# Performance work log

Hardware: AMD Instinct MI355X
Metric: run time of the kernel (lower is better)

## Reference

```python
import jax, jax.numpy as jnp
import numpy as np

E, D, H, K, DIL, T = 8, 768, 3072, 3, 1, 16384


def _conv1d(x, w, b, dilation):
    # x: [1, C_in, L]; w: [C_out, C_in, K]; torch Conv1d with SAME padding
    pad = dilation * (w.shape[-1] - 1) // 2
    y = jax.lax.conv_general_dilated(
        x, w, window_strides=(1,), padding=[(pad, pad)],
        rhs_dilation=(dilation,), dimension_numbers=("NCH", "OIH", "NCH"))
    return y + b[None, :, None]


def setup_inputs() -> dict:
    key = jax.random.key(0)
    k0, k1, k2, k3, k4 = jax.random.split(key, 5)
    inp = jax.random.normal(k0, (T, D), dtype=jnp.float32)
    fwd_expert_count = jnp.full((E,), T // E, dtype=jnp.int32)
    w1 = jax.random.normal(k1, (E, H, D, K), dtype=jnp.float32) * (1.0 / np.sqrt(D * K))
    b1 = jax.random.normal(k2, (E, H), dtype=jnp.float32) * 0.01
    w2 = jax.random.normal(k3, (E, D, H, K), dtype=jnp.float32) * (1.0 / np.sqrt(H * K))
    b2 = jax.random.normal(k4, (E, D), dtype=jnp.float32) * 0.01
    return {"inp": inp, "fwd_expert_count": fwd_expert_count,
            "w1": w1, "b1": b1, "w2": w2, "b2": b2}


def reference(inp, fwd_expert_count, w1, b1, w2, b2):
    # counts define static per-expert segment lengths (constants w.r.t. compute graph)
    counts = np.asarray(jax.device_get(fwd_expert_count))
    x = inp.T[None]  # [1, D, T]
    outs, idx = [], 0
    for i in range(counts.shape[0]):
        n = int(counts[i])
        if n > 0:
            outs.append(_conv1d(x[:, :, idx:idx + n], w1[i], b1[i], DIL))
            idx += n
    h = jax.nn.gelu(jnp.concatenate(outs, axis=2), approximate=False)  # [1, H, T]
    outs, idx = [], 0
    for i in range(counts.shape[0]):
        n = int(counts[i])
        if n > 0:
            outs.append(_conv1d(h[:, :, idx:idx + n], w2[i], b2[i], DIL))
            idx += n
    y = jnp.concatenate(outs, axis=2)[0]  # [D, T]
    return y.T  # [T, D]
```

## Files before the change

### kernel.cpp

```cpp
#include <hip/hip_runtime.h>
#include <hip/hip_bf16.h>
#include <cstdint>

#define E_   8
#define D_   768
#define H_   3072
#define T_   16384
#define SEG  2048
#define PSEG (SEG + 2)

typedef __attribute__((ext_vector_type(8))) __bf16 bf16x8;
typedef __attribute__((ext_vector_type(4))) float f32x4;
typedef __attribute__((ext_vector_type(4))) unsigned int u32x4;

__device__ inline unsigned short f2bf(float f) {
  union { float f; unsigned int u; } v; v.f = f;
  unsigned int u = v.u;
  u += 0x7fffu + ((u >> 16) & 1u);
  return (unsigned short)(u >> 16);
}

__device__ inline float gelu_fast(float x) {
  const float a = -2.302118131f;
  const float b = -0.102944213f;
  float z = x * __builtin_fmaf(b, x * x, a);
  float e = __builtin_amdgcn_exp2f(z);
  return x * __builtin_amdgcn_rcpf(1.0f + e);
}

__device__ inline void gload16(const unsigned short* g, unsigned short* l) {
  __builtin_amdgcn_global_load_lds(
      (const __attribute__((address_space(1))) unsigned int*)g,
      (__attribute__((address_space(3))) unsigned int*)l, 16, 0, 0);
}

__global__ __launch_bounds__(256) void cvt_x_pad_kernel(const float* __restrict__ in,
                                                        unsigned short* __restrict__ out) {
  const int i = blockIdx.x * 256 + threadIdx.x;
  const int elem = i * 8;
  const int row = elem / D_;
  const int col = elem - row * D_;
  const int prow = (row >> 11) * PSEG + 1 + (row & (SEG - 1));
  const float* p = in + (size_t)row * D_ + col;
  u32x4 v;
#pragma unroll
  for (int j = 0; j < 4; ++j)
    v[j] = (unsigned)f2bf(p[2 * j]) | ((unsigned)f2bf(p[2 * j + 1]) << 16);
  *(u32x4*)(out + (size_t)prow * D_ + col) = v;
}

__global__ __launch_bounds__(256) void zero_guards_kernel(unsigned short* __restrict__ buf,
                                                          int C) {
  const int e = blockIdx.x >> 1;
  const size_t row = (size_t)e * PSEG + (blockIdx.x & 1) * (PSEG - 1);
  for (int c = threadIdx.x; c < C; c += 256) buf[row * C + c] = 0;
}

__global__ __launch_bounds__(256) void cvt_w_kernel(const float* __restrict__ in,
                                                    unsigned short* __restrict__ out,
                                                    int C) {
  int r = blockIdx.x;
  const float* src = in + (size_t)r * C * 3;
  unsigned short* dst = out + (size_t)r * C * 3;
  for (int c = threadIdx.x; c < C; c += 256) {
    float v0 = src[c * 3 + 0], v1 = src[c * 3 + 1], v2 = src[c * 3 + 2];
    dst[0 * C + c] = f2bf(v0);
    dst[1 * C + c] = f2bf(v1);
    dst[2 * C + c] = f2bf(v2);
  }
}

template <int CIN, int COUT, bool DO_GELU>
__global__ __launch_bounds__(512, 2) void conv_gemm8_kernel(
    const unsigned short* __restrict__ A,
    const unsigned short* __restrict__ Bt,
    const float* __restrict__ bias,
    void* __restrict__ Out) {
  __shared__ __align__(16) unsigned short lds[65536];

  constexpr int CSTEPS = CIN / 64;
  constexpr int NT = 3 * CSTEPS;
  constexpr int NTN = COUT / 256;

  const int tid  = threadIdx.x;
  const int wid  = tid >> 6, lane = tid & 63;
  const int wm   = wid >> 2, wn = wid & 3;

  const int bid = blockIdx.x;
  const int e   = bid & 7;
  const int rem = bid >> 3;
  const int mc  = rem / (4 * NTN);
  const int r2  = rem - mc * 4 * NTN;
  const int m0  = (mc * 4 + (r2 & 3)) * 256;
  const int n0  = (r2 >> 2) * 256;

  const int rowoff = tid >> 3;
  const int psrc   = ((lane & 7) ^ (lane >> 3)) * 8;
  const int ko     = (lane >> 4) * 16;
  const int ax     = (lane & 7) << 4;

  const size_t abase = ((size_t)e * PSEG + m0) * CIN;

  f32x4 acc[8][4];
#pragma unroll
  for (int n = 0; n < 4; ++n) {
    const float bv = bias[e * COUT + n0 + wn * 64 + n * 16 + (lane & 15)];
#pragma unroll
    for (int m = 0; m < 8; ++m) acc[m][n] = (f32x4){bv, bv, bv, bv};
  }

#define STAGE_A(kt_, part_) do {                                                     \
    const int ktu_ = (kt_);                                                          \
    const int ktc_ = ktu_ < NT ? ktu_ : NT - 1;    \
    const int k3_  = ktc_ / CSTEPS;                                                  \
    const int c0_  = (ktc_ - k3_ * CSTEPS) * 64;                                     \
    const int buf_ = ktu_ & 1;                                                       \
    _Pragma("unroll")                                                                \
    for (int ii_ = 0; ii_ < 2; ++ii_) {                                              \
      gload16(A + abase + (size_t)(ii_ * 128 + (part_) * 64 + rowoff + k3_) * CIN    \
                  + c0_ + psrc,                                                      \
              (unsigned short*)((char*)lds + buf_ * 32768 + ii_ * 16384 +            \
                                (part_) * 8192 + wid * 1024 + lane * 16));           \
    }                                                                                \
  } while (0)

#define STAGE_B(kt_, h_) do {                                                        \
    const int ktu_ = (kt_);                                                          \
    const int ktc_ = ktu_ < NT ? ktu_ : NT - 1;                                      \
    const int k3_  = ktc_ / CSTEPS;                                                  \
    const int c0_  = (ktc_ - k3_ * CSTEPS) * 64;                                     \
    const int buf_ = ktu_ & 1;                                                       \
    _Pragma("unroll")                                                                \
    for (int ii_ = 0; ii_ < 2; ++ii_) {                                              \
      const int brow_ = n0 + (h_) * 128 + ii_ * 64 + rowoff;                         \
      gload16(Bt + ((size_t)(e * COUT + brow_) * 3 + k3_) * CIN + c0_ + psrc,        \
              (unsigned short*)((char*)lds + 65536 + buf_ * 32768 + (h_) * 16384 +  \
                                ii_ * 8192 + wid * 1024 + lane * 16));               \
    }                                                                                \
  } while (0)

#define FULLBAR() do { asm volatile("" ::: "memory");                                \
                       __builtin_amdgcn_s_barrier();                                 \
                       asm volatile("" ::: "memory"); } while (0)
#define VM6() asm volatile("s_waitcnt vmcnt(6)" ::: "memory")
#define VM8() asm volatile("s_waitcnt vmcnt(8)" ::: "memory")
#define VM_NONE()

#define PHASE(cur_, mq_, s_, RB_, bFa_, STAGE_STMT, VMW_) do {                       \
    const char* Ab_ = (const char*)lds + (cur_) * 32768 + wm * 16384;                \
    if (RB_) {                                                                       \
      const char* Bb_ = (const char*)lds + 65536 + (cur_) * 32768 + (wn >> 1) * 16384; \
      _Pragma("unroll")                                                              \
      for (int n_ = 0; n_ < 4; ++n_)                                                 \
        bFa_[n_] = *(const bf16x8*)(Bb_ +                                            \
            ((wn & 1) * 64 + n_ * 16 + (lane & 15)) * 128 + (((s_) * 64 + ko) ^ ax)); \
    }                                                                                \
    bf16x8 aF_[4];                                                                   \
    _Pragma("unroll")                                                                \
    for (int mi_ = 0; mi_ < 4; ++mi_)                                                \
      aF_[mi_] = *(const bf16x8*)(Ab_ +                                              \
          (((mq_) * 4 + mi_) * 16 + (lane & 15)) * 128 + (((s_) * 64 + ko) ^ ax));   \
    STAGE_STMT;                                                                      \
    VMW_();                                                                          \
    FULLBAR();                                                                       \
    __builtin_amdgcn_s_setprio(1);                                                   \
    _Pragma("unroll")                                                                \
    for (int mi_ = 0; mi_ < 4; ++mi_)                                                \
      _Pragma("unroll")                                                              \
      for (int n_ = 0; n_ < 4; ++n_)                                                 \
        acc[(mq_) * 4 + mi_][n_] = __builtin_amdgcn_mfma_f32_16x16x32_bf16(          \
            aF_[mi_], bFa_[n_], acc[(mq_) * 4 + mi_][n_], 0, 0, 0);                  \
    __builtin_amdgcn_s_setprio(0);                                                   \
  } while (0)

  STAGE_B(0, 0); STAGE_B(0, 1); STAGE_A(0, 0); STAGE_A(0, 1);
  STAGE_B(1, 0); STAGE_B(1, 1);
  VM6();
  FULLBAR();

  bf16x8 bF0[4], bF1[4];
  int kt0 = 0;
#pragma unroll 1
  for (int it = 0; it < NT / 2; ++it, kt0 += 2) {
    PHASE(0, 0, 0, 1, bF0, STAGE_A(kt0 + 1, 0), VM_NONE);  FULLBAR();
    PHASE(0, 0, 1, 1, bF1, STAGE_A(kt0 + 1, 1), VM8);      FULLBAR();
    PHASE(0, 1, 0, 0, bF0, STAGE_B(kt0 + 2, 0), VM_NONE);  FULLBAR();
    PHASE(0, 1, 1, 0, bF1, STAGE_B(kt0 + 2, 1), VM6);      FULLBAR();
    PHASE(1, 0, 0, 1, bF0, STAGE_A(kt0 + 2, 0), VM_NONE);  FULLBAR();
    PHASE(1, 0, 1, 1, bF1, STAGE_A(kt0 + 2, 1), VM8);      FULLBAR();
    PHASE(1, 1, 0, 0, bF0, STAGE_B(kt0 + 3, 0), VM_NONE);  FULLBAR();
    PHASE(1, 1, 1, 0, bF1, STAGE_B(kt0 + 3, 1), VM6);      FULLBAR();
  }

  asm volatile("s_waitcnt vmcnt(0)" ::: "memory");

#undef PHASE
#undef STAGE_A
#undef STAGE_B
#undef FULLBAR
#undef VM6
#undef VM8
#undef VM_NONE

#pragma unroll
  for (int m = 0; m < 8; ++m) {
    const int rowb = m0 + wm * 128 + m * 16 + ((lane >> 4) << 2);
#pragma unroll
    for (int n = 0; n < 4; ++n) {
      const int col = n0 + wn * 64 + n * 16 + (lane & 15);
#pragma unroll
      for (int i = 0; i < 4; ++i) {
        if (DO_GELU) {
          const size_t off = ((size_t)e * PSEG + 1 + rowb + i) * COUT + col;
          ((unsigned short*)Out)[off] = f2bf(gelu_fast(acc[m][n][i]));
        } else {
          const size_t off = ((size_t)e * SEG + rowb + i) * COUT + col;
          ((float*)Out)[off] = acc[m][n][i];
        }
      }
    }
  }
}

extern "C" void kernel_launch(void* const* d_in, const int* in_sizes, int n_in,
                              void* d_out, int out_size, void* d_ws, size_t ws_size,
                              hipStream_t stream) {
  const float* inp = (const float*)d_in[0];
  const float* w1 = (const float*)d_in[2];
  const float* b1 = (const float*)d_in[3];
  const float* w2 = (const float*)d_in[4];
  const float* b2 = (const float*)d_in[5];
  float* out = (float*)d_out;
  char* ws = (char*)d_ws;

  const size_t szXp = (size_t)E_ * PSEG * D_ * 2;
  const size_t szHp = (size_t)E_ * PSEG * H_ * 2;
  const size_t szW1 = (size_t)E_ * H_ * 3 * D_ * 2;
  const size_t szW2 = (size_t)E_ * D_ * 3 * H_ * 2;

  unsigned short* Xp  = (unsigned short*)ws;
  unsigned short* Hp  = (unsigned short*)(ws + szXp);
  unsigned short* W1T = (unsigned short*)(ws + szXp + szHp);
  unsigned short* W2T = (unsigned short*)(ws + szXp + szHp + szW1);

  if (ws_size < szXp + szHp + szW1 + szW2) return;

  zero_guards_kernel<<<E_ * 2, 256, 0, stream>>>(Xp, D_);
  zero_guards_kernel<<<E_ * 2, 256, 0, stream>>>(Hp, H_);
  cvt_x_pad_kernel<<<T_ * D_ / 8 / 256, 256, 0, stream>>>(inp, Xp);
  cvt_w_kernel<<<E_ * H_, 256, 0, stream>>>(w1, W1T, D_);
  cvt_w_kernel<<<E_ * D_, 256, 0, stream>>>(w2, W2T, H_);

  constexpr int NWG1 = (H_ / 256) * (SEG / 256) * E_;
  constexpr int NWG2 = (D_ / 256) * (SEG / 256) * E_;
  conv_gemm8_kernel<D_, H_, true>
      <<<NWG1, 512, 0, stream>>>(Xp, W1T, b1, Hp);
  conv_gemm8_kernel<H_, D_, false>
      <<<NWG2, 512, 0, stream>>>(Hp, W2T, b2, out);
}
```

Baseline: 572.8 us.

## Software-pipeline LDS fragment reads one phase ahead of MFMA compute

```diff
diff --git a/kernel.cpp b/kernel.cpp
--- a/kernel.cpp
+++ b/kernel.cpp
@@ -143,34 +143,38 @@
                        __builtin_amdgcn_s_barrier();                                 \
                        asm volatile("" ::: "memory"); } while (0)
 #define VM6() asm volatile("s_waitcnt vmcnt(6)" ::: "memory")
-#define VM8() asm volatile("s_waitcnt vmcnt(8)" ::: "memory")
+#define VM4() asm volatile("s_waitcnt vmcnt(4)" ::: "memory")
 #define VM_NONE()
 
-#define PHASE(cur_, mq_, s_, RB_, bFa_, STAGE_STMT, VMW_) do {                       \
-    const char* Ab_ = (const char*)lds + (cur_) * 32768 + wm * 16384;                \
+#define RA(buf_, mq_, s_, raA_, raB_, RB_) do {                                      \
+    const char* Ab_ = (const char*)lds + (buf_) * 32768 + wm * 16384;                \
     if (RB_) {                                                                       \
-      const char* Bb_ = (const char*)lds + 65536 + (cur_) * 32768 + (wn >> 1) * 16384; \
+      const char* Bb_ = (const char*)lds + 65536 + (buf_) * 32768 + (wn >> 1) * 16384; \
       _Pragma("unroll")                                                              \
       for (int n_ = 0; n_ < 4; ++n_)                                                 \
-        bFa_[n_] = *(const bf16x8*)(Bb_ +                                            \
+        raB_[n_] = *(const bf16x8*)(Bb_ +                                            \
             ((wn & 1) * 64 + n_ * 16 + (lane & 15)) * 128 + (((s_) * 64 + ko) ^ ax)); \
     }                                                                                \
-    bf16x8 aF_[4];                                                                   \
     _Pragma("unroll")                                                                \
     for (int mi_ = 0; mi_ < 4; ++mi_)                                                \
-      aF_[mi_] = *(const bf16x8*)(Ab_ +                                              \
+      raA_[mi_] = *(const bf16x8*)(Ab_ +                                             \
           (((mq_) * 4 + mi_) * 16 + (lane & 15)) * 128 + (((s_) * 64 + ko) ^ ax));   \
+  } while (0)
+
+#define PHASE(raBuf_, raMq_, raS_, raA_, raB_, RB_, useA_, useB_, mq_, STAGE_STMT, VMW_) \
+  do {                                                                               \
+    FULLBAR();                                                                       \
+    RA(raBuf_, raMq_, raS_, raA_, raB_, RB_);                                        \
     STAGE_STMT;                                                                      \
-    VMW_();                                                                          \
-    FULLBAR();                                                                       \
     __builtin_amdgcn_s_setprio(1);                                                   \
     _Pragma("unroll")                                                                \
     for (int mi_ = 0; mi_ < 4; ++mi_)                                                \
       _Pragma("unroll")                                                              \
       for (int n_ = 0; n_ < 4; ++n_)                                                 \
         acc[(mq_) * 4 + mi_][n_] = __builtin_amdgcn_mfma_f32_16x16x32_bf16(          \
-            aF_[mi_], bFa_[n_], acc[(mq_) * 4 + mi_][n_], 0, 0, 0);                  \
+            useA_[mi_], useB_[n_], acc[(mq_) * 4 + mi_][n_], 0, 0, 0);               \
     __builtin_amdgcn_s_setprio(0);                                                   \
+    VMW_();                                                                          \
   } while (0)
 
   STAGE_B(0, 0); STAGE_B(0, 1); STAGE_A(0, 0); STAGE_A(0, 1);
@@ -178,28 +182,31 @@
   VM6();
   FULLBAR();
 
-  bf16x8 bF0[4], bF1[4];
+  bf16x8 aFA[4], aFB[4], bFA[4], bFB[4];
+  RA(0, 0, 0, aFA, bFA, 1);
+
   int kt0 = 0;
 #pragma unroll 1
   for (int it = 0; it < NT / 2; ++it, kt0 += 2) {
-    PHASE(0, 0, 0, 1, bF0, STAGE_A(kt0 + 1, 0), VM_NONE);  FULLBAR();
-    PHASE(0, 0, 1, 1, bF1, STAGE_A(kt0 + 1, 1), VM8);      FULLBAR();
-    PHASE(0, 1, 0, 0, bF0, STAGE_B(kt0 + 2, 0), VM_NONE);  FULLBAR();
-    PHASE(0, 1, 1, 0, bF1, STAGE_B(kt0 + 2, 1), VM6);      FULLBAR();
-    PHASE(1, 0, 0, 1, bF0, STAGE_A(kt0 + 2, 0), VM_NONE);  FULLBAR();
-    PHASE(1, 0, 1, 1, bF1, STAGE_A(kt0 + 2, 1), VM8);      FULLBAR();
-    PHASE(1, 1, 0, 0, bF0, STAGE_B(kt0 + 3, 0), VM_NONE);  FULLBAR();
-    PHASE(1, 1, 1, 0, bF1, STAGE_B(kt0 + 3, 1), VM6);      FULLBAR();
+    PHASE(0,    0,   1,   aFB, bFB, 1, aFA, bFA, 0, STAGE_A(kt0 + 1, 0), VM6);
+    PHASE(0,    1,   0,   aFA, bFA, 0, aFB, bFB, 0, STAGE_A(kt0 + 1, 1), VM_NONE);
+    PHASE(0,    1,   1,   aFB, bFB, 0, aFA, bFA, 1, STAGE_B(kt0 + 2, 0), VM4);
+    PHASE(1,    0,   0,   aFA, bFA, 1, aFB, bFB, 1, STAGE_B(kt0 + 2, 1), VM_NONE);
+    PHASE(1,    0,   1,   aFB, bFB, 1, aFA, bFA, 0, STAGE_A(kt0 + 2, 0), VM6);
+    PHASE(1,    1,   0,   aFA, bFA, 0, aFB, bFB, 0, STAGE_A(kt0 + 2, 1), VM_NONE);
+    PHASE(1,    1,   1,   aFB, bFB, 0, aFA, bFA, 1, STAGE_B(kt0 + 3, 0), VM4);
+    PHASE(0,    0,   0,   aFA, bFA, 1, aFB, bFB, 1, STAGE_B(kt0 + 3, 1), VM_NONE);
   }
 
   asm volatile("s_waitcnt vmcnt(0)" ::: "memory");
 
 #undef PHASE
+#undef RA
 #undef STAGE_A
 #undef STAGE_B
 #undef FULLBAR
 #undef VM6
-#undef VM8
+#undef VM4
 #undef VM_NONE
 
 #pragma unroll
```

New measurement: 552.4 us. -3.6%, faster.
